# Performance work log

Hardware: AMD Instinct MI355X
Metric: run time of the kernel (lower is better)

Reference implementation:

```python
import jax, jax.numpy as jnp
import numpy as np
from jax import lax

SMOOTH = 1e-06
SKEL_ITERS = 10  # thresh_width in the original soft_skeletonize


def _maxpool3(x):
    # 3x3 max pool, stride 1, padding 1 on NCHW
    return lax.reduce_window(
        x, -jnp.inf, lax.max,
        window_dimensions=(1, 1, 3, 3),
        window_strides=(1, 1, 1, 1),
        padding=((0, 0), (0, 0), (1, 1), (1, 1)))


def soft_skeletonize(x):
    def body(i, x):
        min_pool_x = -_maxpool3(-x)                      # 3x3 min-pool (erosion)
        contour = jax.nn.relu(_maxpool3(min_pool_x) - min_pool_x)
        return jax.nn.relu(x - contour)
    return lax.fori_loop(0, SKEL_ITERS, body, x)


def norm_intersection(center_line, vessel):
    B, C = center_line.shape[:2]
    clf = center_line.reshape(B, C, -1)
    vf = vessel.reshape(B, C, -1)
    intersection = jnp.sum(clf * vf, axis=-1)
    return (intersection + SMOOTH) / (jnp.sum(clf, axis=-1) + SMOOTH)


def setup_inputs() -> dict:
    key = jax.random.key(0)
    k1, k2 = jax.random.split(key)
    B, C, H, W = 32, 1, 512, 512
    pred = jax.random.uniform(k1, (B, C, H, W), dtype=jnp.float32)
    target = (jax.random.uniform(k2, (B, C, H, W), dtype=jnp.float32) > 0.85).astype(jnp.float32)
    return {"pred": pred, "target": target}


def reference(pred, target):
    cl_pred = soft_skeletonize(pred)
    target_skeleton = soft_skeletonize(target)
    iflat = norm_intersection(cl_pred, target)
    tflat = norm_intersection(target_skeleton, pred)
    intersection = jnp.sum(iflat * tflat)
    return 1.0 - 2.0 * intersection / jnp.sum(iflat + tflat)
```

## Files before the change

kernel.cpp:

```cpp
#include <hip/hip_runtime.h>
#include <hip/hip_fp16.h>
#include <math.h>

#define HH 512
#define WW 512
#define BB 32
#define CHUNK 32

typedef unsigned u32;

#define NEG_INF2 0xFC00FC00u
#define POS_INF2 0x7C007C00u

__device__ __forceinline__ u32 pkmin(u32 a, u32 b) {
    u32 r; asm("v_pk_min_f16 %0, %1, %2" : "=v"(r) : "v"(a), "v"(b)); return r;
}
__device__ __forceinline__ u32 pkmax(u32 a, u32 b) {
    u32 r; asm("v_pk_max_f16 %0, %1, %2" : "=v"(r) : "v"(a), "v"(b)); return r;
}
__device__ __forceinline__ u32 pksub(u32 a, u32 b) {
    u32 r; asm("v_pk_add_f16 %0, %1, %2 neg_lo:[0,1] neg_hi:[0,1]" : "=v"(r) : "v"(a), "v"(b)); return r;
}
__device__ __forceinline__ u32 min3p(u32 a, u32 b, u32 c) { return pkmin(pkmin(a, b), c); }
__device__ __forceinline__ u32 max3p(u32 a, u32 b, u32 c) { return pkmax(pkmax(a, b), c); }

__device__ __forceinline__ u32 shl1(u32 a, u32 b) {
    return __builtin_amdgcn_alignbit(b, a, 16);
}

union H2U { __half2 h; u32 u; };
__device__ __forceinline__ u32 f2toh2(float lo, float hi) {
    H2U t; t.h = __float22half2_rn(make_float2(lo, hi)); return t.u;
}
__device__ __forceinline__ float2 h2tof2(u32 v) {
    H2U t; t.u = v; return __half22float2(t.h);
}

template <int F32>
__device__ __forceinline__ void loadrow6(const float* __restrict__ imgF,
                                         const unsigned short* __restrict__ imgH,
                                         int R, int cm4, int c0, int cp4,
                                         bool isL, bool isR, u32* X) {
    const int Rc = R < 0 ? 0 : (R > HH - 1 ? HH - 1 : R);
    if (F32) {
        const float* rb = imgF + (size_t)Rc * WW;
        float4 v0 = *(const float4*)(rb + cm4);
        float4 v1 = *(const float4*)(rb + c0);
        float4 v2 = *(const float4*)(rb + cp4);
        X[0] = f2toh2(v0.x, v0.y); X[1] = f2toh2(v0.z, v0.w);
        X[2] = f2toh2(v1.x, v1.y); X[3] = f2toh2(v1.z, v1.w);
        X[4] = f2toh2(v2.x, v2.y); X[5] = f2toh2(v2.z, v2.w);
    } else {
        const unsigned short* rb = imgH + (size_t)Rc * WW;
        uint2 a = *(const uint2*)(rb + cm4);
        uint2 b = *(const uint2*)(rb + c0);
        uint2 c = *(const uint2*)(rb + cp4);
        X[0] = a.x; X[1] = a.y; X[2] = b.x; X[3] = b.y; X[4] = c.x; X[5] = c.y;
    }
    u32 fl = __builtin_amdgcn_perm(X[0], X[1], 0x05040100u);
    X[1] = isL ? fl : X[1];
    u32 fr = __builtin_amdgcn_perm(X[4], X[3], 0x07060302u);
    X[4] = isR ? fr : X[4];
}

template <int SRCF32, int FUSED>
__device__ __forceinline__ void rowstep(
    const float* __restrict__ imgF, const unsigned short* __restrict__ imgH,
    const float* __restrict__ cmp, unsigned short* __restrict__ outp,
    float& acc0, float& acc1,
    int R, int cm4, int gx0, int cp4, bool isL, bool isR, bool doStore,
    u32 (&X)[6], u32 (&XL)[6],
    u32 (&hm0o)[6], u32 (&hm0n)[6], u32 (&mn0p)[4],
    u32 (&hx0o)[4], u32 (&hx0n)[4],
    u32 (&x0o)[4], u32 (&x0n)[4],
    u32 (&hm1o)[4], u32 (&hm1n)[4], u32 (&mn1p)[2],
    u32 (&hx1o)[2], u32 (&hx1n)[2],
    u32 (&x1o)[2], u32 (&x1n)[2],
    const u32 (&mk)[8],
    float4& cqC, float4& cqL) {
    loadrow6<SRCF32>(imgF, imgH, R + 3, cm4, gx0, cp4, isL, isR, XL);

    float4 cmpCur;
    if (FUSED) {
        cmpCur = cqC;
        int Rc = R - 1;
        Rc = Rc < 0 ? 0 : (Rc > HH - 1 ? HH - 1 : Rc);
        cqL = *(const float4*)(cmp + (size_t)Rc * WW + gx0);
    }

    u32 L[7];
    L[0] = shl1(X[0], X[0]);
    #pragma unroll
    for (int j = 1; j <= 5; ++j) L[j] = shl1(X[j - 1], X[j]);
    L[6] = shl1(X[5], X[5]);
    u32 hm0c[6];
    #pragma unroll
    for (int j = 0; j < 6; ++j) hm0c[j] = min3p(L[j], X[j], L[j + 1]);

    u32 M[6];
    #pragma unroll
    for (int j = 0; j < 6; ++j) M[j] = min3p(hm0o[j], hm0n[j], hm0c[j]);
    if (!((unsigned)(R - 1) < HH)) {
        #pragma unroll
        for (int j = 0; j < 6; ++j) M[j] = NEG_INF2;
    }
    M[0] = pkmin(M[0], mk[0]); M[1] = pkmin(M[1], mk[1]);
    M[4] = pkmin(M[4], mk[2]); M[5] = pkmin(M[5], mk[3]);

    u32 ML[6];
    #pragma unroll
    for (int j = 1; j <= 5; ++j) ML[j] = shl1(M[j - 1], M[j]);
    u32 hx0c[4];
    #pragma unroll
    for (int j = 0; j < 4; ++j) hx0c[j] = max3p(ML[j + 1], M[j + 1], ML[j + 2]);

    u32 x1c[4];
    #pragma unroll
    for (int j = 0; j < 4; ++j) {
        u32 mp = max3p(hx0o[j], hx0n[j], hx0c[j]);
        u32 ct = pkmax(pksub(mp, mn0p[j]), 0u);
        x1c[j] = pkmax(pksub(x0o[j], ct), 0u);
    }
    if (!((unsigned)(R - 2) < HH)) {
        #pragma unroll
        for (int j = 0; j < 4; ++j) x1c[j] = POS_INF2;
    }
    x1c[0] = pkmax(x1c[0], mk[4]);
    x1c[3] = pkmax(x1c[3], mk[5]);

    #pragma unroll
    for (int j = 0; j < 6; ++j) hm0o[j] = hm0c[j];
    #pragma unroll
    for (int j = 0; j < 4; ++j) { mn0p[j] = M[j + 1]; hx0o[j] = hx0c[j]; x0o[j] = X[j + 1]; }

    u32 XL1[5];
    XL1[0] = shl1(x1c[0], x1c[0]);
    #pragma unroll
    for (int j = 1; j <= 3; ++j) XL1[j] = shl1(x1c[j - 1], x1c[j]);
    XL1[4] = shl1(x1c[3], x1c[3]);
    u32 hm1c[4];
    #pragma unroll
    for (int j = 0; j < 4; ++j) hm1c[j] = min3p(XL1[j], x1c[j], XL1[j + 1]);

    u32 M1[4];
    #pragma unroll
    for (int j = 0; j < 4; ++j) M1[j] = min3p(hm1o[j], hm1n[j], hm1c[j]);
    if (!((unsigned)(R - 3) < HH)) {
        #pragma unroll
        for (int j = 0; j < 4; ++j) M1[j] = NEG_INF2;
    }
    M1[0] = pkmin(M1[0], mk[6]);
    M1[3] = pkmin(M1[3], mk[7]);

    u32 M1s[4];
    #pragma unroll
    for (int j = 1; j <= 3; ++j) M1s[j] = shl1(M1[j - 1], M1[j]);
    u32 hx1c[2];
    hx1c[0] = max3p(M1s[1], M1[1], M1s[2]);
    hx1c[1] = max3p(M1s[2], M1[2], M1s[3]);

    if (doStore) {
        u32 o[2];
        #pragma unroll
        for (int k = 0; k < 2; ++k) {
            u32 mp = max3p(hx1o[k], hx1n[k], hx1c[k]);
            u32 ct = pkmax(pksub(mp, mn1p[k]), 0u);
            o[k] = pkmax(pksub(x1o[k], ct), 0u);
        }
        if (FUSED) {
            float2 f0 = h2tof2(o[0]);
            float2 f1 = h2tof2(o[1]);
            acc0 += f0.x * cmpCur.x + f0.y * cmpCur.y + f1.x * cmpCur.z + f1.y * cmpCur.w;
            acc1 += f0.x + f0.y + f1.x + f1.y;
        } else {
            uint2 ov;
            ov.x = o[0]; ov.y = o[1];
            *(uint2*)(outp + (size_t)(R - 4) * WW + gx0) = ov;
        }
    }

    #pragma unroll
    for (int j = 0; j < 4; ++j) hm1o[j] = hm1c[j];
    mn1p[0] = M1[1]; mn1p[1] = M1[2];
    hx1o[0] = hx1c[0]; hx1o[1] = hx1c[1];
    x1o[0] = x1c[1]; x1o[1] = x1c[2];
}

template <int SRCF32, int FUSED>
__global__ __launch_bounds__(256) void skel2h_t(const float* __restrict__ sfA,
                                                const float* __restrict__ sfB,
                                                const unsigned short* __restrict__ shA,
                                                const unsigned short* __restrict__ shB,
                                                const float* __restrict__ cmpA,
                                                const float* __restrict__ cmpB,
                                                unsigned short* __restrict__ dst,
                                                float* __restrict__ partials) {
    const int s = blockIdx.x * 64 + threadIdx.x;
    const int y0 = (blockIdx.y * 4 + threadIdx.y) * CHUNK;
    const int z = blockIdx.z;
    const float* imgF = nullptr;
    const unsigned short* imgH = nullptr;
    if (SRCF32) imgF = (z < BB) ? (sfA + (size_t)z * (HH * WW))
                                : (sfB + (size_t)(z - BB) * (HH * WW));
    else        imgH = (z < BB) ? (shA + (size_t)z * (HH * WW))
                                : (shB + (size_t)(z - BB) * (HH * WW));
    const float* cmp = nullptr;
    if (FUSED) cmp = (z < BB) ? (cmpA + (size_t)z * (HH * WW))
                              : (cmpB + (size_t)(z - BB) * (HH * WW));
    unsigned short* outp = FUSED ? nullptr : (dst + (size_t)z * (HH * WW));
    const int gx0 = 4 * s;
    const bool isL = (s == 0), isR = (s == 127);
    const int cm4 = isL ? 0 : gx0 - 4;
    const int cp4 = isR ? gx0 : gx0 + 4;

    u32 mk[8];
    mk[0] = isL ? 0xFC007C00u : POS_INF2;
    mk[1] = isL ? NEG_INF2    : POS_INF2;
    mk[2] = isR ? NEG_INF2    : POS_INF2;
    mk[3] = isR ? 0x7C00FC00u : POS_INF2;
    mk[4] = isL ? POS_INF2    : NEG_INF2;
    mk[5] = isR ? POS_INF2    : NEG_INF2;
    mk[6] = isL ? 0xFC007C00u : POS_INF2;
    mk[7] = isR ? 0x7C00FC00u : POS_INF2;

    u32 hm0a[6], hm0b[6], mn0p[4];
    u32 hx0a[4], hx0b[4], x0a[4], x0b[4];
    u32 hm1a[4], hm1b[4], mn1p[2];
    u32 hx1a[2], hx1b[2], x1a[2], x1b[2];
    u32 xs0[6], xs1[6], xs2[6], xs3[6];
    float4 cq0, cq1, cq2, cq3;

    #pragma unroll
    for (int j = 0; j < 6; ++j) { hm0a[j] = POS_INF2; hm0b[j] = POS_INF2; }
    #pragma unroll
    for (int j = 0; j < 4; ++j) {
        mn0p[j] = NEG_INF2; hx0a[j] = NEG_INF2; hx0b[j] = NEG_INF2;
        x0a[j] = POS_INF2; x0b[j] = POS_INF2;
        hm1a[j] = POS_INF2; hm1b[j] = POS_INF2;
    }
    #pragma unroll
    for (int k = 0; k < 2; ++k) {
        mn1p[k] = NEG_INF2; hx1a[k] = NEG_INF2; hx1b[k] = NEG_INF2;
        x1a[k] = POS_INF2; x1b[k] = POS_INF2;
    }
    cq0.x = cq0.y = cq0.z = cq0.w = 0.f;
    cq1 = cq0; cq2 = cq0; cq3 = cq0;

    float acc0 = 0.0f, acc1 = 0.0f;

    loadrow6<SRCF32>(imgF, imgH, y0 - 4, cm4, gx0, cp4, isL, isR, xs0);
    loadrow6<SRCF32>(imgF, imgH, y0 - 3, cm4, gx0, cp4, isL, isR, xs1);
    loadrow6<SRCF32>(imgF, imgH, y0 - 2, cm4, gx0, cp4, isL, isR, xs2);

    #pragma unroll 1
    for (int it = 0; it < (CHUNK + 8) / 4; ++it) {
        const int Rb = y0 - 4 + 4 * it;
        const bool doStore = (it >= 2);
        rowstep<SRCF32, FUSED>(imgF, imgH, cmp, outp, acc0, acc1,
            Rb + 0, cm4, gx0, cp4, isL, isR, doStore,
            xs0, xs3, hm0a, hm0b, mn0p, hx0a, hx0b, x0a, x0b,
            hm1a, hm1b, mn1p, hx1a, hx1b, x1a, x1b, mk, cq0, cq3);
        rowstep<SRCF32, FUSED>(imgF, imgH, cmp, outp, acc0, acc1,
            Rb + 1, cm4, gx0, cp4, isL, isR, doStore,
            xs1, xs0, hm0b, hm0a, mn0p, hx0b, hx0a, x0b, x0a,
            hm1b, hm1a, mn1p, hx1b, hx1a, x1b, x1a, mk, cq1, cq0);
        rowstep<SRCF32, FUSED>(imgF, imgH, cmp, outp, acc0, acc1,
            Rb + 2, cm4, gx0, cp4, isL, isR, doStore,
            xs2, xs1, hm0a, hm0b, mn0p, hx0a, hx0b, x0a, x0b,
            hm1a, hm1b, mn1p, hx1a, hx1b, x1a, x1b, mk, cq2, cq1);
        rowstep<SRCF32, FUSED>(imgF, imgH, cmp, outp, acc0, acc1,
            Rb + 3, cm4, gx0, cp4, isL, isR, doStore,
            xs3, xs2, hm0b, hm0a, mn0p, hx0b, hx0a, x0b, x0a,
            hm1b, hm1a, mn1p, hx1b, hx1a, x1b, x1a, mk, cq3, cq2);
    }

    if (FUSED) {
        for (int off = 32; off; off >>= 1) {
            acc0 += __shfl_down(acc0, off);
            acc1 += __shfl_down(acc1, off);
        }
        __shared__ float red[4][2];
        if (threadIdx.x == 0) { red[threadIdx.y][0] = acc0; red[threadIdx.y][1] = acc1; }
        __syncthreads();
        if (threadIdx.x == 0 && threadIdx.y == 0) {
            const int tile = blockIdx.x * gridDim.y + blockIdx.y;
            float* p = partials + ((size_t)z * 16 + tile) * 2;
            p[0] = red[0][0] + red[1][0] + red[2][0] + red[3][0];
            p[1] = red[0][1] + red[1][1] + red[2][1] + red[3][1];
        }
    }
}

__global__ __launch_bounds__(64) void finalize2(const float* __restrict__ partials,
                                                int ntiles,
                                                float* __restrict__ out) {
    const int b = threadIdx.x;
    float iflat = 0.f, tflat = 0.f;
    if (b < BB) {
        float v0 = 0.f, v1 = 0.f, v2 = 0.f, v3 = 0.f;
        for (int t = 0; t < ntiles; ++t) {
            v0 += partials[((size_t)b * 16 + t) * 2 + 0];
            v1 += partials[((size_t)b * 16 + t) * 2 + 1];
            v2 += partials[((size_t)(b + BB) * 16 + t) * 2 + 0];
            v3 += partials[((size_t)(b + BB) * 16 + t) * 2 + 1];
        }
        iflat = (v0 + 1e-6f) / (v1 + 1e-6f);
        tflat = (v2 + 1e-6f) / (v3 + 1e-6f);
    }
    float prod = iflat * tflat;
    float ssum = iflat + tflat;
    for (int off = 32; off; off >>= 1) {
        prod += __shfl_down(prod, off);
        ssum += __shfl_down(ssum, off);
    }
    if (threadIdx.x == 0) out[0] = 1.0f - 2.0f * prod / ssum;
}

extern "C" void kernel_launch(void* const* d_in, const int* in_sizes, int n_in,
                              void* d_out, int out_size, void* d_ws, size_t ws_size,
                              hipStream_t stream) {
    const float* pred = (const float*)d_in[0];
    const float* target = (const float*)d_in[1];
    float* out = (float*)d_out;
    char* ws = (char*)d_ws;
    const size_t N = (size_t)HH * WW;
    const size_t HALF = (size_t)BB * N;
    const size_t IMG16 = HALF * sizeof(unsigned short);

    dim3 block(64, 4);
    const int nby = HH / (CHUNK * 4);
    const int ntiles = 2 * nby;

    if (ws_size >= 4 * IMG16 + (1 << 16)) {
        unsigned short* A = (unsigned short*)ws;
        unsigned short* B = (unsigned short*)(ws + 2 * IMG16);
        float* partials = (float*)(ws + 4 * IMG16);
        dim3 grid(2, nby, 2 * BB);
        skel2h_t<1, 0><<<grid, block, 0, stream>>>(pred, target, nullptr, nullptr,
                                                   nullptr, nullptr, A, nullptr);
        skel2h_t<0, 0><<<grid, block, 0, stream>>>(nullptr, nullptr, A, A + HALF,
                                                   nullptr, nullptr, B, nullptr);
        skel2h_t<0, 0><<<grid, block, 0, stream>>>(nullptr, nullptr, B, B + HALF,
                                                   nullptr, nullptr, A, nullptr);
        skel2h_t<0, 0><<<grid, block, 0, stream>>>(nullptr, nullptr, A, A + HALF,
                                                   nullptr, nullptr, B, nullptr);
        skel2h_t<0, 1><<<grid, block, 0, stream>>>(nullptr, nullptr, B, B + HALF,
                                                   target, pred, nullptr, partials);
        finalize2<<<1, 64, 0, stream>>>(partials, ntiles, out);
    } else {
        unsigned short* b0 = (unsigned short*)ws;
        unsigned short* b1 = (unsigned short*)(ws + IMG16);
        float* partials = (float*)(ws + 2 * IMG16);
        dim3 grid(2, nby, BB);
        skel2h_t<1, 0><<<grid, block, 0, stream>>>(pred, pred, nullptr, nullptr,
                                                   nullptr, nullptr, b0, nullptr);
        skel2h_t<0, 0><<<grid, block, 0, stream>>>(nullptr, nullptr, b0, b0,
                                                   nullptr, nullptr, b1, nullptr);
        skel2h_t<0, 0><<<grid, block, 0, stream>>>(nullptr, nullptr, b1, b1,
                                                   nullptr, nullptr, b0, nullptr);
        skel2h_t<0, 0><<<grid, block, 0, stream>>>(nullptr, nullptr, b0, b0,
                                                   nullptr, nullptr, b1, nullptr);
        skel2h_t<0, 1><<<grid, block, 0, stream>>>(nullptr, nullptr, b1, b1,
                                                   target, target, nullptr, partials);
        skel2h_t<1, 0><<<grid, block, 0, stream>>>(target, target, nullptr, nullptr,
                                                   nullptr, nullptr, b0, nullptr);
        skel2h_t<0, 0><<<grid, block, 0, stream>>>(nullptr, nullptr, b0, b0,
                                                   nullptr, nullptr, b1, nullptr);
        skel2h_t<0, 0><<<grid, block, 0, stream>>>(nullptr, nullptr, b1, b1,
                                                   nullptr, nullptr, b0, nullptr);
        skel2h_t<0, 0><<<grid, block, 0, stream>>>(nullptr, nullptr, b0, b0,
                                                   nullptr, nullptr, b1, nullptr);
        skel2h_t<0, 1><<<grid, block, 0, stream>>>(nullptr, nullptr, b1, b1,
                                                   pred, pred, nullptr,
                                                   partials + (size_t)BB * 16 * 2);
        finalize2<<<1, 64, 0, stream>>>(partials, ntiles, out);
    }
}
```

Before: 143.4 us.

## Fuse three skeleton iterations per kernel pass with wider halo

Adds a kernel that applies three soft-skeleton iterations in one pass, using a 6-row and wider column halo held in registers. The schedule goes from five two-iteration passes to two three-iteration passes plus two of the existing two-iteration passes. This removes one full fp16 image round trip through memory and one launch per image set. In exchange each thread does redundant halo work, loads 10 words per row instead of 6, and holds far more live registers, which may hurt occupancy.

```diff
diff --git a/kernel.cpp b/kernel.cpp
--- a/kernel.cpp
+++ b/kernel.cpp
@@ -23,7 +23,6 @@
 }
 __device__ __forceinline__ u32 min3p(u32 a, u32 b, u32 c) { return pkmin(pkmin(a, b), c); }
 __device__ __forceinline__ u32 max3p(u32 a, u32 b, u32 c) { return pkmax(pkmax(a, b), c); }
-
 __device__ __forceinline__ u32 shl1(u32 a, u32 b) {
     return __builtin_amdgcn_alignbit(b, a, 16);
 }
@@ -173,8 +172,7 @@
             acc0 += f0.x * cmpCur.x + f0.y * cmpCur.y + f1.x * cmpCur.z + f1.y * cmpCur.w;
             acc1 += f0.x + f0.y + f1.x + f1.y;
         } else {
-            uint2 ov;
-            ov.x = o[0]; ov.y = o[1];
+            uint2 ov; ov.x = o[0]; ov.y = o[1];
             *(uint2*)(outp + (size_t)(R - 4) * WW + gx0) = ov;
         }
     }
@@ -291,6 +289,283 @@
     }
 }
 
+template <int F32>
+__device__ __forceinline__ void loadrow10(const float* __restrict__ imgF,
+                                          const unsigned short* __restrict__ imgH,
+                                          int R, const int (&pb)[5],
+                                          const u32 (&xm)[8], u32 (&X)[10]) {
+    const int Rc = R < 0 ? 0 : (R > HH - 1 ? HH - 1 : R);
+    if (F32) {
+        const float* rb = imgF + (size_t)Rc * WW;
+        #pragma unroll
+        for (int m = 0; m < 5; ++m) {
+            float4 v = *(const float4*)(rb + 2 * pb[m]);
+            X[2 * m] = f2toh2(v.x, v.y); X[2 * m + 1] = f2toh2(v.z, v.w);
+        }
+    } else {
+        const unsigned short* rb = imgH + (size_t)Rc * WW;
+        #pragma unroll
+        for (int m = 0; m < 5; ++m) {
+            uint2 v = *(const uint2*)(rb + 2 * pb[m]);
+            X[2 * m] = v.x; X[2 * m + 1] = v.y;
+        }
+    }
+    X[0] = pkmax(X[0], xm[0]); X[1] = pkmax(X[1], xm[1]);
+    X[2] = pkmax(X[2], xm[2]); X[3] = pkmax(X[3], xm[3]);
+    X[6] = pkmax(X[6], xm[4]); X[7] = pkmax(X[7], xm[5]);
+    X[8] = pkmax(X[8], xm[6]); X[9] = pkmax(X[9], xm[7]);
+}
+
+template <int SRCF32>
+__device__ __forceinline__ void rowstep3(
+    const float* __restrict__ imgF, const unsigned short* __restrict__ imgH,
+    unsigned short* __restrict__ outp,
+    int R, int gx0, bool doStore,
+    const int (&pb)[5], const u32 (&xm)[8], const u32 (&m0)[6],
+    const u32 (&x1m)[4], const u32 (&mk)[8],
+    const u32 (&X)[10], u32 (&XL)[10],
+    u32 (&hm0o)[8], u32 (&hm0n)[8], u32 (&mn0p)[6],
+    u32 (&hx0o)[6], u32 (&hx0n)[6], u32 (&x0o)[6], u32 (&x0n)[6],
+    u32 (&hm1o)[6], u32 (&hm1n)[6], u32 (&mn1p)[4],
+    u32 (&hx1o)[4], u32 (&hx1n)[4], u32 (&x1o)[4], u32 (&x1n)[4],
+    u32 (&hm2o)[4], u32 (&hm2n)[4], u32 (&mn2p)[2],
+    u32 (&hx2o)[2], u32 (&hx2n)[2], u32 (&x2o)[2], u32 (&x2n)[2]) {
+    loadrow10<SRCF32>(imgF, imgH, R + 3, pb, xm, XL);
+
+    u32 L[10];
+    #pragma unroll
+    for (int j = 1; j <= 9; ++j) L[j] = shl1(X[j - 1], X[j]);
+    u32 hm0[8];
+    #pragma unroll
+    for (int a = 0; a < 8; ++a) hm0[a] = min3p(L[a + 1], X[a + 1], L[a + 2]);
+    u32 M0[8];
+    #pragma unroll
+    for (int a = 0; a < 8; ++a) M0[a] = min3p(hm0o[a], hm0n[a], hm0[a]);
+    if (!((unsigned)(R - 1) < HH)) {
+        #pragma unroll
+        for (int a = 0; a < 8; ++a) M0[a] = NEG_INF2;
+    }
+    M0[0] = pkmin(M0[0], m0[0]); M0[1] = pkmin(M0[1], m0[1]); M0[2] = pkmin(M0[2], m0[2]);
+    M0[5] = pkmin(M0[5], m0[3]); M0[6] = pkmin(M0[6], m0[4]); M0[7] = pkmin(M0[7], m0[5]);
+    u32 ML[8];
+    #pragma unroll
+    for (int a = 1; a <= 7; ++a) ML[a] = shl1(M0[a - 1], M0[a]);
+    u32 hx0[6];
+    #pragma unroll
+    for (int b = 0; b < 6; ++b) hx0[b] = max3p(ML[b + 1], M0[b + 1], ML[b + 2]);
+    u32 x1c[6];
+    #pragma unroll
+    for (int b = 0; b < 6; ++b) {
+        u32 mp = max3p(hx0o[b], hx0n[b], hx0[b]);
+        u32 ct = pkmax(pksub(mp, mn0p[b]), 0u);
+        x1c[b] = pkmax(pksub(x0o[b], ct), 0u);
+    }
+    if (!((unsigned)(R - 2) < HH)) {
+        #pragma unroll
+        for (int b = 0; b < 6; ++b) x1c[b] = POS_INF2;
+    }
+    x1c[0] = pkmax(x1c[0], x1m[0]); x1c[1] = pkmax(x1c[1], x1m[1]);
+    x1c[4] = pkmax(x1c[4], x1m[2]); x1c[5] = pkmax(x1c[5], x1m[3]);
+    #pragma unroll
+    for (int a = 0; a < 8; ++a) hm0o[a] = hm0[a];
+    #pragma unroll
+    for (int b = 0; b < 6; ++b) { mn0p[b] = M0[b + 1]; hx0o[b] = hx0[b]; x0o[b] = X[b + 2]; }
+
+    u32 L1[7];
+    L1[0] = shl1(x1c[0], x1c[0]);
+    #pragma unroll
+    for (int j = 1; j <= 5; ++j) L1[j] = shl1(x1c[j - 1], x1c[j]);
+    L1[6] = shl1(x1c[5], x1c[5]);
+    u32 hm1[6];
+    #pragma unroll
+    for (int j = 0; j < 6; ++j) hm1[j] = min3p(L1[j], x1c[j], L1[j + 1]);
+    u32 M1[6];
+    #pragma unroll
+    for (int j = 0; j < 6; ++j) M1[j] = min3p(hm1o[j], hm1n[j], hm1[j]);
+    if (!((unsigned)(R - 3) < HH)) {
+        #pragma unroll
+        for (int j = 0; j < 6; ++j) M1[j] = NEG_INF2;
+    }
+    M1[0] = pkmin(M1[0], mk[0]); M1[1] = pkmin(M1[1], mk[1]);
+    M1[4] = pkmin(M1[4], mk[2]); M1[5] = pkmin(M1[5], mk[3]);
+    u32 ML1[6];
+    #pragma unroll
+    for (int j = 1; j <= 5; ++j) ML1[j] = shl1(M1[j - 1], M1[j]);
+    u32 hx1[4];
+    #pragma unroll
+    for (int b = 0; b < 4; ++b) hx1[b] = max3p(ML1[b + 1], M1[b + 1], ML1[b + 2]);
+    u32 x2c[4];
+    #pragma unroll
+    for (int b = 0; b < 4; ++b) {
+        u32 mp = max3p(hx1o[b], hx1n[b], hx1[b]);
+        u32 ct = pkmax(pksub(mp, mn1p[b]), 0u);
+        x2c[b] = pkmax(pksub(x1o[b], ct), 0u);
+    }
+    if (!((unsigned)(R - 4) < HH)) {
+        #pragma unroll
+        for (int b = 0; b < 4; ++b) x2c[b] = POS_INF2;
+    }
+    x2c[0] = pkmax(x2c[0], mk[4]);
+    x2c[3] = pkmax(x2c[3], mk[5]);
+    #pragma unroll
+    for (int j = 0; j < 6; ++j) hm1o[j] = hm1[j];
+    #pragma unroll
+    for (int b = 0; b < 4; ++b) { mn1p[b] = M1[b + 1]; hx1o[b] = hx1[b]; x1o[b] = x1c[b + 1]; }
+
+    u32 L2[5];
+    L2[0] = shl1(x2c[0], x2c[0]);
+    #pragma unroll
+    for (int j = 1; j <= 3; ++j) L2[j] = shl1(x2c[j - 1], x2c[j]);
+    L2[4] = shl1(x2c[3], x2c[3]);
+    u32 hm2[4];
+    #pragma unroll
+    for (int j = 0; j < 4; ++j) hm2[j] = min3p(L2[j], x2c[j], L2[j + 1]);
+    u32 M2[4];
+    #pragma unroll
+    for (int j = 0; j < 4; ++j) M2[j] = min3p(hm2o[j], hm2n[j], hm2[j]);
+    if (!((unsigned)(R - 5) < HH)) {
+        #pragma unroll
+        for (int j = 0; j < 4; ++j) M2[j] = NEG_INF2;
+    }
+    M2[0] = pkmin(M2[0], mk[6]);
+    M2[3] = pkmin(M2[3], mk[7]);
+    u32 ML2[4];
+    #pragma unroll
+    for (int j = 1; j <= 3; ++j) ML2[j] = shl1(M2[j - 1], M2[j]);
+    u32 hx2[2];
+    hx2[0] = max3p(ML2[1], M2[1], ML2[2]);
+    hx2[1] = max3p(ML2[2], M2[2], ML2[3]);
+    if (doStore) {
+        u32 o[2];
+        #pragma unroll
+        for (int k = 0; k < 2; ++k) {
+            u32 mp = max3p(hx2o[k], hx2n[k], hx2[k]);
+            u32 ct = pkmax(pksub(mp, mn2p[k]), 0u);
+            o[k] = pkmax(pksub(x2o[k], ct), 0u);
+        }
+        uint2 ov; ov.x = o[0]; ov.y = o[1];
+        *(uint2*)(outp + (size_t)(R - 6) * WW + gx0) = ov;
+    }
+    #pragma unroll
+    for (int j = 0; j < 4; ++j) hm2o[j] = hm2[j];
+    mn2p[0] = M2[1]; mn2p[1] = M2[2];
+    hx2o[0] = hx2[0]; hx2o[1] = hx2[1];
+    x2o[0] = x2c[1]; x2o[1] = x2c[2];
+}
+
+template <int SRCF32>
+__global__ __launch_bounds__(256) void skel3h(const float* __restrict__ sfA,
+                                              const float* __restrict__ sfB,
+                                              const unsigned short* __restrict__ shA,
+                                              const unsigned short* __restrict__ shB,
+                                              unsigned short* __restrict__ dst) {
+    const int s = blockIdx.x * 64 + threadIdx.x;
+    const int y0 = (blockIdx.y * 4 + threadIdx.y) * CHUNK;
+    const int z = blockIdx.z;
+    const float* imgF = nullptr;
+    const unsigned short* imgH = nullptr;
+    if (SRCF32) imgF = (z < BB) ? (sfA + (size_t)z * (HH * WW))
+                                : (sfB + (size_t)(z - BB) * (HH * WW));
+    else        imgH = (z < BB) ? (shA + (size_t)z * (HH * WW))
+                                : (shB + (size_t)(z - BB) * (HH * WW));
+    unsigned short* outp = dst + (size_t)z * (HH * WW);
+    const int gx0 = 4 * s;
+    const int pl = 2 * s;
+    const bool isL = (s == 0), isR = (s == 127);
+
+    int pb[5];
+    #pragma unroll
+    for (int m = 0; m < 5; ++m) {
+        int b = pl - 4 + 2 * m;
+        pb[m] = b < 0 ? 0 : (b > 254 ? 254 : b);
+    }
+    u32 xm[8];
+    xm[0] = (s <= 1)   ? POS_INF2 : NEG_INF2;
+    xm[1] = (s <= 1)   ? POS_INF2 : NEG_INF2;
+    xm[2] = (s == 0)   ? POS_INF2 : NEG_INF2;
+    xm[3] = (s == 0)   ? POS_INF2 : NEG_INF2;
+    xm[4] = (s == 127) ? POS_INF2 : NEG_INF2;
+    xm[5] = (s == 127) ? POS_INF2 : NEG_INF2;
+    xm[6] = (s >= 126) ? POS_INF2 : NEG_INF2;
+    xm[7] = (s >= 126) ? POS_INF2 : NEG_INF2;
+    u32 m0[6];
+    m0[0] = (s <= 1)   ? NEG_INF2 : POS_INF2;
+    m0[1] = (s == 0)   ? NEG_INF2 : POS_INF2;
+    m0[2] = (s == 0)   ? NEG_INF2 : POS_INF2;
+    m0[3] = (s == 127) ? NEG_INF2 : POS_INF2;
+    m0[4] = (s == 127) ? NEG_INF2 : POS_INF2;
+    m0[5] = (s >= 126) ? NEG_INF2 : POS_INF2;
+    u32 x1m[4];
+    x1m[0] = (s == 0)   ? POS_INF2 : NEG_INF2;
+    x1m[1] = (s == 0)   ? POS_INF2 : NEG_INF2;
+    x1m[2] = (s == 127) ? POS_INF2 : NEG_INF2;
+    x1m[3] = (s == 127) ? POS_INF2 : NEG_INF2;
+    u32 mk[8];
+    mk[0] = isL ? 0xFC007C00u : POS_INF2;
+    mk[1] = isL ? NEG_INF2    : POS_INF2;
+    mk[2] = isR ? NEG_INF2    : POS_INF2;
+    mk[3] = isR ? 0x7C00FC00u : POS_INF2;
+    mk[4] = isL ? POS_INF2    : NEG_INF2;
+    mk[5] = isR ? POS_INF2    : NEG_INF2;
+    mk[6] = isL ? 0xFC007C00u : POS_INF2;
+    mk[7] = isR ? 0x7C00FC00u : POS_INF2;
+
+    u32 hm0a[8], hm0b[8], mn0p[6];
+    u32 hx0a[6], hx0b[6], x0a[6], x0b[6];
+    u32 hm1a[6], hm1b[6], mn1p[4];
+    u32 hx1a[4], hx1b[4], x1a[4], x1b[4];
+    u32 hm2a[4], hm2b[4], mn2p[2];
+    u32 hx2a[2], hx2b[2], x2a[2], x2b[2];
+    u32 xs0[10], xs1[10], xs2[10], xs3[10];
+
+    #pragma unroll
+    for (int j = 0; j < 8; ++j) { hm0a[j] = POS_INF2; hm0b[j] = POS_INF2; }
+    #pragma unroll
+    for (int j = 0; j < 6; ++j) {
+        mn0p[j] = NEG_INF2; hx0a[j] = NEG_INF2; hx0b[j] = NEG_INF2;
+        x0a[j] = POS_INF2; x0b[j] = POS_INF2;
+        hm1a[j] = POS_INF2; hm1b[j] = POS_INF2;
+    }
+    #pragma unroll
+    for (int j = 0; j < 4; ++j) {
+        mn1p[j] = NEG_INF2; hx1a[j] = NEG_INF2; hx1b[j] = NEG_INF2;
+        x1a[j] = POS_INF2; x1b[j] = POS_INF2;
+        hm2a[j] = POS_INF2; hm2b[j] = POS_INF2;
+    }
+    #pragma unroll
+    for (int k = 0; k < 2; ++k) {
+        mn2p[k] = NEG_INF2; hx2a[k] = NEG_INF2; hx2b[k] = NEG_INF2;
+        x2a[k] = POS_INF2; x2b[k] = POS_INF2;
+    }
+
+    const int R0 = y0 - 6;
+    loadrow10<SRCF32>(imgF, imgH, R0 + 0, pb, xm, xs0);
+    loadrow10<SRCF32>(imgF, imgH, R0 + 1, pb, xm, xs1);
+    loadrow10<SRCF32>(imgF, imgH, R0 + 2, pb, xm, xs2);
+
+    #pragma unroll 1
+    for (int it = 0; it < (CHUNK + 12) / 4; ++it) {
+        const int Rb = R0 + 4 * it;
+        const bool st = (it >= 3);
+        rowstep3<SRCF32>(imgF, imgH, outp, Rb + 0, gx0, st, pb, xm, m0, x1m, mk,
+            xs0, xs3, hm0a, hm0b, mn0p, hx0a, hx0b, x0a, x0b,
+            hm1a, hm1b, mn1p, hx1a, hx1b, x1a, x1b,
+            hm2a, hm2b, mn2p, hx2a, hx2b, x2a, x2b);
+        rowstep3<SRCF32>(imgF, imgH, outp, Rb + 1, gx0, st, pb, xm, m0, x1m, mk,
+            xs1, xs0, hm0b, hm0a, mn0p, hx0b, hx0a, x0b, x0a,
+            hm1b, hm1a, mn1p, hx1b, hx1a, x1b, x1a,
+            hm2b, hm2a, mn2p, hx2b, hx2a, x2b, x2a);
+        rowstep3<SRCF32>(imgF, imgH, outp, Rb + 2, gx0, st, pb, xm, m0, x1m, mk,
+            xs2, xs1, hm0a, hm0b, mn0p, hx0a, hx0b, x0a, x0b,
+            hm1a, hm1b, mn1p, hx1a, hx1b, x1a, x1b,
+            hm2a, hm2b, mn2p, hx2a, hx2b, x2a, x2b);
+        rowstep3<SRCF32>(imgF, imgH, outp, Rb + 3, gx0, st, pb, xm, m0, x1m, mk,
+            xs3, xs2, hm0b, hm0a, mn0p, hx0b, hx0a, x0b, x0a,
+            hm1b, hm1a, mn1p, hx1b, hx1a, x1b, x1a,
+            hm2b, hm2a, mn2p, hx2b, hx2a, x2b, x2a);
+    }
+}
+
 __global__ __launch_bounds__(64) void finalize2(const float* __restrict__ partials,
                                                 int ntiles,
                                                 float* __restrict__ out) {
@@ -336,15 +611,11 @@
         unsigned short* B = (unsigned short*)(ws + 2 * IMG16);
         float* partials = (float*)(ws + 4 * IMG16);
         dim3 grid(2, nby, 2 * BB);
-        skel2h_t<1, 0><<<grid, block, 0, stream>>>(pred, target, nullptr, nullptr,
-                                                   nullptr, nullptr, A, nullptr);
-        skel2h_t<0, 0><<<grid, block, 0, stream>>>(nullptr, nullptr, A, A + HALF,
-                                                   nullptr, nullptr, B, nullptr);
+        skel3h<1><<<grid, block, 0, stream>>>(pred, target, nullptr, nullptr, A);
+        skel3h<0><<<grid, block, 0, stream>>>(nullptr, nullptr, A, A + HALF, B);
         skel2h_t<0, 0><<<grid, block, 0, stream>>>(nullptr, nullptr, B, B + HALF,
                                                    nullptr, nullptr, A, nullptr);
-        skel2h_t<0, 0><<<grid, block, 0, stream>>>(nullptr, nullptr, A, A + HALF,
-                                                   nullptr, nullptr, B, nullptr);
-        skel2h_t<0, 1><<<grid, block, 0, stream>>>(nullptr, nullptr, B, B + HALF,
+        skel2h_t<0, 1><<<grid, block, 0, stream>>>(nullptr, nullptr, A, A + HALF,
                                                    target, pred, nullptr, partials);
         finalize2<<<1, 64, 0, stream>>>(partials, ntiles, out);
     } else {
@@ -352,25 +623,17 @@
         unsigned short* b1 = (unsigned short*)(ws + IMG16);
         float* partials = (float*)(ws + 2 * IMG16);
         dim3 grid(2, nby, BB);
-        skel2h_t<1, 0><<<grid, block, 0, stream>>>(pred, pred, nullptr, nullptr,
-                                                   nullptr, nullptr, b0, nullptr);
-        skel2h_t<0, 0><<<grid, block, 0, stream>>>(nullptr, nullptr, b0, b0,
-                                                   nullptr, nullptr, b1, nullptr);
+        skel3h<1><<<grid, block, 0, stream>>>(pred, pred, nullptr, nullptr, b0);
+        skel3h<0><<<grid, block, 0, stream>>>(nullptr, nullptr, b0, b0, b1);
         skel2h_t<0, 0><<<grid, block, 0, stream>>>(nullptr, nullptr, b1, b1,
                                                    nullptr, nullptr, b0, nullptr);
-        skel2h_t<0, 0><<<grid, block, 0, stream>>>(nullptr, nullptr, b0, b0,
-                                                   nullptr, nullptr, b1, nullptr);
-        skel2h_t<0, 1><<<grid, block, 0, stream>>>(nullptr, nullptr, b1, b1,
+        skel2h_t<0, 1><<<grid, block, 0, stream>>>(nullptr, nullptr, b0, b0,
                                                    target, target, nullptr, partials);
-        skel2h_t<1, 0><<<grid, block, 0, stream>>>(target, target, nullptr, nullptr,
-                                                   nullptr, nullptr, b0, nullptr);
-        skel2h_t<0, 0><<<grid, block, 0, stream>>>(nullptr, nullptr, b0, b0,
-                                                   nullptr, nullptr, b1, nullptr);
+        skel3h<1><<<grid, block, 0, stream>>>(target, target, nullptr, nullptr, b0);
+        skel3h<0><<<grid, block, 0, stream>>>(nullptr, nullptr, b0, b0, b1);
         skel2h_t<0, 0><<<grid, block, 0, stream>>>(nullptr, nullptr, b1, b1,
                                                    nullptr, nullptr, b0, nullptr);
-        skel2h_t<0, 0><<<grid, block, 0, stream>>>(nullptr, nullptr, b0, b0,
-                                                   nullptr, nullptr, b1, nullptr);
-        skel2h_t<0, 1><<<grid, block, 0, stream>>>(nullptr, nullptr, b1, b1,
+        skel2h_t<0, 1><<<grid, block, 0, stream>>>(nullptr, nullptr, b0, b0,
                                                    pred, pred, nullptr,
                                                    partials + (size_t)BB * 16 * 2);
         finalize2<<<1, 64, 0, stream>>>(partials, ntiles, out);
```

After: 170.6 us. 19.0% more time.
